# Kernel optimization log

Measured on AMD Instinct MI355X. Metric: run time of the kernel, lower is better.

Reference implementation:

```python
import jax, jax.numpy as jnp
import numpy as np
import math

B, S = 1, 2048
HID = 2048
H = 16
Q_LORA = 1536
KV_LORA = 512
ROPE_D = 64
NOPE_D = 128
V_D = 128
Q_HD = NOPE_D + ROPE_D  # 192
THETA = 10000.0
EPS = 1e-6


def rmsnorm(x, w):
    xf = x.astype(jnp.float32)
    n = xf * jax.lax.rsqrt(jnp.mean(xf * xf, axis=-1, keepdims=True) + EPS)
    return n.astype(x.dtype) * w


def rotate_half(x):
    d = x.shape[-1] // 2
    return jnp.concatenate([-x[..., d:], x[..., :d]], axis=-1)


def setup_inputs() -> dict:
    key = jax.random.key(0)
    ks = jax.random.split(key, 8)
    std = 0.02
    x = jax.random.normal(ks[0], (B, S, HID), dtype=jnp.float32)
    position = jnp.broadcast_to(jnp.arange(S, dtype=jnp.int32), (B, S))
    mask = jnp.broadcast_to(jnp.tril(jnp.ones((S, S), dtype=jnp.int32)), (B, S, S))
    Wq_down = jax.random.normal(ks[1], (HID, Q_LORA), dtype=jnp.float32) * std
    q_norm_w = jnp.ones((Q_LORA,), dtype=jnp.float32)
    Wq_up = jax.random.normal(ks[2], (Q_LORA, H * Q_HD), dtype=jnp.float32) * std
    Wkv_down = jax.random.normal(ks[3], (HID, KV_LORA + ROPE_D), dtype=jnp.float32) * std
    kv_norm_w = jnp.ones((KV_LORA,), dtype=jnp.float32)
    Wkv_up = jax.random.normal(ks[4], (KV_LORA, H * (NOPE_D + V_D)), dtype=jnp.float32) * std
    Wout = jax.random.normal(ks[5], (HID, HID), dtype=jnp.float32) * std
    return {"x": x, "position": position, "mask": mask,
            "Wq_down": Wq_down, "q_norm_w": q_norm_w, "Wq_up": Wq_up,
            "Wkv_down": Wkv_down, "kv_norm_w": kv_norm_w, "Wkv_up": Wkv_up,
            "Wout": Wout}


def reference(x, position, mask, Wq_down, q_norm_w, Wq_up, Wkv_down, kv_norm_w, Wkv_up, Wout):
    b, s, _ = x.shape
    # --- Q path: low-rank down -> RMSNorm -> up ---
    q = rmsnorm(x @ Wq_down, q_norm_w) @ Wq_up            # [B,S,H*Q_HD]
    q = q.reshape(b, s, H, Q_HD).transpose(0, 2, 1, 3)    # [B,H,S,Q_HD]
    q_nope, q_rope = q[..., :NOPE_D], q[..., NOPE_D:]
    # --- KV path ---
    c = x @ Wkv_down                                       # [B,S,KV_LORA+ROPE_D]
    c_kv, k_rope = c[..., :KV_LORA], c[..., KV_LORA:]
    kv = rmsnorm(c_kv, kv_norm_w) @ Wkv_up                 # [B,S,H*(NOPE_D+V_D)]
    kv = kv.reshape(b, s, H, NOPE_D + V_D).transpose(0, 2, 1, 3)
    k_nope, v_state = kv[..., :NOPE_D], kv[..., NOPE_D:]
    k_rope = k_rope[:, None]                               # [B,1,S,ROPE_D]
    # --- RoPE (decoupled, on rope dims only) ---
    inv_freq = 1.0 / (THETA ** (jnp.arange(0, ROPE_D, 2, dtype=jnp.float32) / ROPE_D))
    t = jnp.arange(s, dtype=jnp.float32)
    freqs = jnp.outer(t, inv_freq)                         # [S,ROPE_D/2]
    emb = jnp.concatenate([freqs, freqs], axis=-1)         # [S,ROPE_D]
    cos = jnp.cos(emb)[position][:, None]                  # [B,1,S,ROPE_D]
    sin = jnp.sin(emb)[position][:, None]
    q_rope = q_rope * cos + rotate_half(q_rope) * sin      # [B,H,S,ROPE_D]
    k_rope = k_rope * cos + rotate_half(k_rope) * sin      # [B,1,S,ROPE_D]
    k_rope = jnp.broadcast_to(k_rope, (b, H, s, ROPE_D))
    q_state = jnp.concatenate([q_nope, q_rope], axis=-1)   # [B,H,S,Q_HD]
    k_state = jnp.concatenate([k_nope, k_rope], axis=-1)   # [B,H,S,Q_HD]
    # --- attention (note: original scales by sqrt(v_head_dim)) ---
    scores = jnp.einsum('bhqd,bhkd->bhqk', q_state, k_state) / math.sqrt(V_D)
    scores = jnp.where(mask[:, None] == 0, -jnp.inf, scores)
    att_w = jax.nn.softmax(scores, axis=-1)
    att = jnp.einsum('bhqk,bhkd->bhqd', att_w, v_state)    # [B,H,S,V_D]
    att = att.transpose(0, 2, 1, 3).reshape(b, s, H * V_D) # [B,S,HID]
    return att @ Wout
```

## Files before the change

### kernel.cpp

```cpp
#include <hip/hip_runtime.h>
#include <hip/hip_bf16.h>
#include <math.h>

typedef __bf16 bf16_t;
typedef __bf16 bf16x4 __attribute__((ext_vector_type(4)));
typedef __bf16 bf16x8 __attribute__((ext_vector_type(8)));
typedef float f32x4 __attribute__((ext_vector_type(4)));

#define LOG2E 1.4426950408889634f

typedef const __attribute__((address_space(1))) void* as1cv;
typedef __attribute__((address_space(3))) void* as3v;

__device__ __forceinline__ void gload16(const bf16_t* g, bf16_t* l) {
  __builtin_amdgcn_global_load_lds((as1cv)g, (as3v)l, 16, 0, 0);
}

__global__ __launch_bounds__(256)
void prep_k(const float* __restrict__ x, const float* __restrict__ Wqd,
            const float* __restrict__ Wkvd, const float* __restrict__ Wqu,
            const float* __restrict__ Wkvu, const float* __restrict__ Wout,
            bf16_t* __restrict__ xb, bf16_t* __restrict__ WdT,
            bf16_t* __restrict__ WquT, bf16_t* __restrict__ WkvuT,
            bf16_t* __restrict__ WoutT) {
  __shared__ float t[32][33];
  const int tid = threadIdx.x;
  int bid = blockIdx.x;
  if (bid < 4096) {
    int i = (bid * 256 + tid) * 4;
    float4 v = *(const float4*)(x + i);
    bf16x4 o;
    o[0] = (bf16_t)v.x; o[1] = (bf16_t)v.y; o[2] = (bf16_t)v.z; o[3] = (bf16_t)v.w;
    *(bf16x4*)(xb + i) = o;
    return;
  }
  bid -= 4096;
  const float* in; bf16_t* out; int C, R, bx, by;
  if (bid < 3072)       { in = Wqd;  out = WdT;           R = 2048; C = 1536; bx = bid % 48;  by = bid / 48; }
  else if (bid < 4224)  { int b = bid - 3072;  in = Wkvd; out = WdT + 3145728; R = 2048; C = 576;  bx = b % 18;  by = b / 18; }
  else if (bid < 8832)  { int b = bid - 4224;  in = Wqu;  out = WquT;  R = 1536; C = 3072; bx = b % 96;  by = b / 96; }
  else if (bid < 10880) { int b = bid - 8832;  in = Wkvu; out = WkvuT; R = 512;  C = 4096; bx = b % 128; by = b / 128; }
  else                  { int b = bid - 10880; in = Wout; out = WoutT; R = 2048; C = 2048; bx = b % 64;  by = b / 64; }
  const int c0 = bx * 32, r0 = by * 32;
  const int tx = tid & 31, ty = tid >> 5;
#pragma unroll
  for (int i = 0; i < 32; i += 8)
    t[ty + i][tx] = in[(size_t)(r0 + ty + i) * C + c0 + tx];
  __syncthreads();
#pragma unroll
  for (int i = 0; i < 32; i += 8)
    out[(size_t)(c0 + ty + i) * R + r0 + tx] = (bf16_t)t[tx][ty + i];
}


__device__ __forceinline__ void stage8(const bf16_t* __restrict__ A,
                                       const bf16_t* __restrict__ Bt,
                                       int K, int N, int m0, int n0, int k0,
                                       bf16_t* As, bf16_t* Bs,
                                       int wave, int srow, int scol) {
#pragma unroll
  for (int i = 0; i < 2; ++i) {
    int r0 = (wave * 2 + i) * 8;
    gload16(A + (size_t)(m0 + r0 + srow) * K + k0 + scol, As + r0 * 64);
    int br = n0 + r0 + srow;
    if (br >= N) br = N - 1;
    gload16(Bt + (size_t)br * K + k0 + scol, Bs + r0 * 64);
  }
}

__device__ __forceinline__ void compute8(const bf16_t* As, const bf16_t* Bs,
                                         f32x4 (&acc)[2][4],
                                         int lane, int wr, int wc) {
  const int lm = lane & 15;
  const int sw = lm & 7;
#pragma unroll
  for (int ks = 0; ks < 2; ++ks) {
    const int ck = ((lane >> 4) + ks * 4) ^ sw;
    bf16x8 af[2], bfr[4];
#pragma unroll
    for (int i = 0; i < 2; ++i)
      af[i] = *(const bf16x8*)(As + (wr + i * 16 + lm) * 64 + ck * 8);
#pragma unroll
    for (int i = 0; i < 4; ++i)
      bfr[i] = *(const bf16x8*)(Bs + (wc + i * 16 + lm) * 64 + ck * 8);
#pragma unroll
    for (int mi = 0; mi < 2; ++mi)
#pragma unroll
      for (int ni = 0; ni < 4; ++ni)
        acc[mi][ni] = __builtin_amdgcn_mfma_f32_16x16x32_bf16(
            af[mi], bfr[ni], acc[mi][ni], 0, 0, 0);
  }
}

#define VMCNT(n) asm volatile("s_waitcnt vmcnt(" #n ")" ::: "memory")

__device__ __forceinline__ void gemm128_dbuf8(const bf16_t* __restrict__ A,
                                              const bf16_t* __restrict__ Bt,
                                              int K, int N, int m0, int n0,
                                              bf16_t* lds, f32x4 (&acc)[2][4],
                                              int wave, int lane) {
  const int srow = lane >> 3;
  const int scol = ((lane & 7) ^ srow) * 8;
  const int wr = (wave >> 1) * 32, wc = (wave & 1) * 64;
  bf16_t* A0 = lds;
  bf16_t* B0 = lds + 8192;
  bf16_t* A1 = lds + 16384;
  bf16_t* B1 = lds + 24576;
  const int nk = K >> 6;
  stage8(A, Bt, K, N, m0, n0, 0, A0, B0, wave, srow, scol);
  stage8(A, Bt, K, N, m0, n0, 64, A1, B1, wave, srow, scol);
  VMCNT(4);
  __builtin_amdgcn_s_barrier();
#pragma unroll 1
  for (int t = 0; t < nk; t += 2) {
    compute8(A0, B0, acc, lane, wr, wc);
    __builtin_amdgcn_s_barrier();
    if (t + 2 < nk) {
      stage8(A, Bt, K, N, m0, n0, (t + 2) << 6, A0, B0, wave, srow, scol);
      VMCNT(4);
    } else {
      VMCNT(0);
    }
    __builtin_amdgcn_s_barrier();
    compute8(A1, B1, acc, lane, wr, wc);
    if (t + 3 <= nk) {
      __builtin_amdgcn_s_barrier();
      if (t + 3 < nk) {
        stage8(A, Bt, K, N, m0, n0, (t + 3) << 6, A1, B1, wave, srow, scol);
        VMCNT(4);
      } else {
        VMCNT(0);
      }
      __builtin_amdgcn_s_barrier();
    }
  }
}

__global__ __launch_bounds__(512)
void gemm_dn8(const bf16_t* __restrict__ A, const bf16_t* __restrict__ Bt,
              bf16_t* __restrict__ C, int M, int N, int K) {
  __shared__ __align__(16) bf16_t lds[32768];
  const int tid = threadIdx.x;
  const int wave = tid >> 6, lane = tid & 63;
  const int m0 = blockIdx.y * 128, n0 = blockIdx.x * 128;
  const int wr = (wave >> 1) * 32, wc = (wave & 1) * 64;
  f32x4 acc[2][4] = {};
  gemm128_dbuf8(A, Bt, K, N, m0, n0, lds, acc, wave, lane);
  const int lm = lane & 15, lr = (lane >> 4) * 4;
#pragma unroll
  for (int mi = 0; mi < 2; ++mi)
#pragma unroll
    for (int ni = 0; ni < 4; ++ni) {
      int col = n0 + wc + ni * 16 + lm;
      if (col < N) {
#pragma unroll
        for (int i = 0; i < 4; ++i) {
          int row = m0 + wr + mi * 16 + lr + i;
          C[(size_t)row * N + col] = (bf16_t)acc[mi][ni][i];
        }
      }
    }
}

__global__ __launch_bounds__(512)
void gemm_outf8(const bf16_t* __restrict__ A, const bf16_t* __restrict__ Bt,
                float* __restrict__ C, int M, int N, int K) {
  __shared__ __align__(16) bf16_t lds[32768];
  const int tid = threadIdx.x;
  const int wave = tid >> 6, lane = tid & 63;
  const int m0 = blockIdx.y * 128, n0 = blockIdx.x * 128;
  const int wr = (wave >> 1) * 32, wc = (wave & 1) * 64;
  f32x4 acc[2][4] = {};
  gemm128_dbuf8(A, Bt, K, N, m0, n0, lds, acc, wave, lane);
  const int lm = lane & 15, lr = (lane >> 4) * 4;
#pragma unroll
  for (int mi = 0; mi < 2; ++mi)
#pragma unroll
    for (int ni = 0; ni < 4; ++ni) {
      int col = n0 + wc + ni * 16 + lm;
#pragma unroll
      for (int i = 0; i < 4; ++i) {
        int row = m0 + wr + mi * 16 + lr + i;
        C[(size_t)row * N + col] = acc[mi][ni][i];
      }
    }
}

__global__ __launch_bounds__(512)
void gemm_qkvup8(const bf16_t* __restrict__ qdn, const bf16_t* __restrict__ WquT,
                 const bf16_t* __restrict__ ckvn, const bf16_t* __restrict__ WkvuT,
                 const int* __restrict__ pos, bf16_t* __restrict__ qs,
                 bf16_t* __restrict__ ks, bf16_t* __restrict__ vt) {
  __shared__ __align__(16) bf16_t lds[32768];
  const int tid = threadIdx.x;
  const int wave = tid >> 6, lane = tid & 63;
  const int m0 = blockIdx.y * 128;
  const int wr = (wave >> 1) * 32, wc = (wave & 1) * 64;
  const int lm = lane & 15, lr = (lane >> 4) * 4;
  f32x4 acc[2][4] = {};
  if (blockIdx.x < 24) {
    const int n0 = blockIdx.x * 128;
    gemm128_dbuf8(qdn, WquT, 1536, 3072, m0, n0, lds, acc, wave, lane);
    const bool rope = (((n0 + wc) / 64) % 3) == 2;
    if (rope) {
#pragma unroll
      for (int mi = 0; mi < 2; ++mi)
#pragma unroll
        for (int i = 0; i < 4; ++i) {
          int row = m0 + wr + mi * 16 + lr + i;
          float p = (float)pos[row];
#pragma unroll
          for (int nl = 0; nl < 2; ++nl) {
            int fi = nl * 16 + lm;
            float ang = p * exp2f(-(float)fi * 0.41524101186092030f);
            float sn, cs;
            sincosf(ang, &sn, &cs);
            float v0 = acc[mi][nl][i], v1 = acc[mi][nl + 2][i];
            int c = n0 + wc + nl * 16 + lm;
            int h = c / 192, d = c - h * 192;
            bf16_t* base = qs + ((size_t)h * 2048 + row) * 192;
            base[d]      = (bf16_t)(v0 * cs - v1 * sn);
            base[d + 32] = (bf16_t)(v1 * cs + v0 * sn);
          }
        }
    } else {
#pragma unroll
      for (int mi = 0; mi < 2; ++mi)
#pragma unroll
        for (int ni = 0; ni < 4; ++ni) {
          int c = n0 + wc + ni * 16 + lm;
          int h = c / 192, d = c - h * 192;
#pragma unroll
          for (int i = 0; i < 4; ++i) {
            int row = m0 + wr + mi * 16 + lr + i;
            qs[((size_t)h * 2048 + row) * 192 + d] = (bf16_t)acc[mi][ni][i];
          }
        }
    }
  } else {
    const int n0 = (blockIdx.x - 24) * 128;
    gemm128_dbuf8(ckvn, WkvuT, 512, 4096, m0, n0, lds, acc, wave, lane);
#pragma unroll
    for (int mi = 0; mi < 2; ++mi)
#pragma unroll
      for (int ni = 0; ni < 4; ++ni) {
        int c = n0 + wc + ni * 16 + lm;
        int h = c >> 8, j = c & 255;
#pragma unroll
        for (int i = 0; i < 4; ++i) {
          int row = m0 + wr + mi * 16 + lr + i;
          bf16_t v = (bf16_t)acc[mi][ni][i];
          if (j < 128)
            ks[((size_t)h * 2048 + row) * 192 + j] = v;
          else
            vt[((size_t)h * 128 + (j - 128)) * 2048 + row] = v;
        }
      }
  }
}

__global__ __launch_bounds__(256)
void normrope_k(const bf16_t* __restrict__ Cd, const float* __restrict__ qnw,
                const float* __restrict__ kvnw, const int* __restrict__ pos,
                bf16_t* __restrict__ qdn, bf16_t* __restrict__ ckvn,
                bf16_t* __restrict__ ks) {
  __shared__ float red[4];
  const int bid = blockIdx.x, tid = threadIdx.x;
  if (bid < 4096) {
    const bf16_t* xr;
    const float* W;
    bf16_t* yr;
    int C;
    if (bid < 2048) {
      xr = Cd + (size_t)bid * 2112; W = qnw; yr = qdn + (size_t)bid * 1536; C = 1536;
    } else {
      int r = bid - 2048;
      xr = Cd + (size_t)r * 2112 + 1536; W = kvnw; yr = ckvn + (size_t)r * 512; C = 512;
    }
    int nch = C >> 3;
    bool act = tid < nch;
    float xv[8];
    float ss = 0.f;
    if (act) {
      bf16x8 v = *(const bf16x8*)(xr + tid * 8);
#pragma unroll
      for (int i = 0; i < 8; ++i) { xv[i] = (float)v[i]; ss += xv[i] * xv[i]; }
    }
#pragma unroll
    for (int off = 1; off < 64; off <<= 1) ss += __shfl_xor(ss, off, 64);
    if ((tid & 63) == 0) red[tid >> 6] = ss;
    __syncthreads();
    float tot = red[0] + red[1] + red[2] + red[3];
    float rs = rsqrtf(tot / (float)C + 1e-6f);
    if (act) {
      bf16x8 o;
#pragma unroll
      for (int i = 0; i < 8; ++i) {
        bf16_t nb = (bf16_t)(xv[i] * rs);
        o[i] = (bf16_t)((float)nb * W[tid * 8 + i]);
      }
      *(bf16x8*)(yr + tid * 8) = o;
    }
  } else {
    int s = bid - 4096, d = tid;
    if (d < 64) {
      float v = (float)Cd[(size_t)s * 2112 + 2048 + d];
      int fi = d & 31;
      float p = (float)pos[s];
      float ang = p * exp2f(-(float)fi * 0.415241011860920295f);
      float sn = sinf(ang), co = cosf(ang);
      float other = (float)Cd[(size_t)s * 2112 + 2048 + (d < 32 ? d + 32 : d - 32)];
      v = (d < 32) ? v * co - other * sn : v * co + other * sn;
      bf16_t bv = (bf16_t)v;
#pragma unroll
      for (int h = 0; h < 16; ++h)
        ks[((size_t)h * 2048 + s) * 192 + 128 + d] = bv;
    }
  }
}

__global__ __launch_bounds__(256)
void attn3_k(const bf16_t* __restrict__ Q, const bf16_t* __restrict__ Kst,
             const bf16_t* __restrict__ Vt, bf16_t* __restrict__ O) {
  __shared__ __align__(16) bf16_t Ks[64 * 192];
  __shared__ __align__(16) bf16_t Vs[144 * 64];
  __shared__ __align__(16) bf16_t Ps[4][16 * 72];
  const int bid = blockIdx.x + (blockIdx.y << 5);
  const int lo = bid & 255;
  const int h = lo >> 4;
  const int j = lo & 15;
  const int t = (bid >> 8) ? j : 31 - j;
  const int q0 = t * 64;
  const int nk = t + 1;
  const int tid = threadIdx.x, wave = tid >> 6, lane = tid & 63;
  const int lm = lane & 15, lg = lane >> 4;
  const bf16_t* Qh = Q + (size_t)h * 2048 * 192;
  const bf16_t* Kh = Kst + (size_t)h * 2048 * 192;
  const bf16_t* Vh = Vt + (size_t)h * 128 * 2048;
  const float sc = 0.08838834764831845f * LOG2E;

  bf16x8 aq[6];
#pragma unroll
  for (int tt = 0; tt < 6; ++tt)
    aq[tt] = *(const bf16x8*)(Qh + (size_t)(q0 + wave * 16 + lm) * 192 + tt * 32 + lg * 8);

#pragma unroll
  for (int jj = 0; jj < 4; ++jj) {
    int idx = jj * 256 + tid;
    Vs[128 * 64 + idx] = (bf16_t)(idx < 64 ? 1.0f : 0.0f);
  }

  int kr[6], kc8[6], vr[4], vc8[4];
#pragma unroll
  for (int jj = 0; jj < 6; ++jj) {
    int s = (wave * 6 + jj) * 64 + lane;
    kr[jj] = s / 24;
    kc8[jj] = ((s % 24) ^ (kr[jj] & 7)) * 8;
  }
#pragma unroll
  for (int jj = 0; jj < 4; ++jj) {
    int s = (wave * 4 + jj) * 64 + lane;
    vr[jj] = s >> 3;
    vc8[jj] = ((s & 7) ^ (vr[jj] & 7)) * 8;
  }

  bf16x8 kstg[6], vstg[4];
#pragma unroll
  for (int jj = 0; jj < 6; ++jj)
    kstg[jj] = *(const bf16x8*)(Kh + (size_t)kr[jj] * 192 + kc8[jj]);
#pragma unroll
  for (int jj = 0; jj < 4; ++jj)
    vstg[jj] = *(const bf16x8*)(Vh + (size_t)vr[jj] * 2048 + vc8[jj]);

  f32x4 o[9] = {};

  for (int kt = 0; kt < nk; ++kt) {
    const int k0 = kt * 64;
    if (kt) __syncthreads();
#pragma unroll
    for (int jj = 0; jj < 6; ++jj)
      *(bf16x8*)(Ks + ((wave * 6 + jj) * 64 + lane) * 8) = kstg[jj];
#pragma unroll
    for (int jj = 0; jj < 4; ++jj)
      *(bf16x8*)(Vs + ((wave * 4 + jj) * 64 + lane) * 8) = vstg[jj];
    __syncthreads();

    if (kt + 1 < nk) {
      const int k1 = k0 + 64;
#pragma unroll
      for (int jj = 0; jj < 6; ++jj)
        kstg[jj] = *(const bf16x8*)(Kh + (size_t)(k1 + kr[jj]) * 192 + kc8[jj]);
#pragma unroll
      for (int jj = 0; jj < 4; ++jj)
        vstg[jj] = *(const bf16x8*)(Vh + (size_t)vr[jj] * 2048 + k1 + vc8[jj]);
    }

    f32x4 sa[4] = {};
    __builtin_amdgcn_s_setprio(1);
#pragma unroll
    for (int ct = 0; ct < 4; ++ct) {
#pragma unroll
      for (int tt = 0; tt < 6; ++tt) {
        int cc = (tt * 4 + lg) ^ (lm & 7);
        bf16x8 bk = *(const bf16x8*)(Ks + (ct * 16 + lm) * 192 + cc * 8);
        sa[ct] = __builtin_amdgcn_mfma_f32_16x16x32_bf16(aq[tt], bk, sa[ct], 0, 0, 0);
      }
    }
    __builtin_amdgcn_s_setprio(0);

    bf16_t* Pw = Ps[wave];
    const bool diag = (kt == nk - 1);
#pragma unroll
    for (int i = 0; i < 4; ++i) {
      const int row = q0 + wave * 16 + lg * 4 + i;
#pragma unroll
      for (int ct = 0; ct < 4; ++ct) {
        float p = exp2f(sa[ct][i] * sc);
        if (diag && (k0 + ct * 16 + lm > row)) p = 0.f;
        Pw[(lg * 4 + i) * 72 + ct * 16 + lm] = (bf16_t)p;
      }
    }
    __builtin_amdgcn_s_waitcnt(0xC07F);

    __builtin_amdgcn_s_setprio(1);
#pragma unroll
    for (int ks2 = 0; ks2 < 2; ++ks2) {
      bf16x8 ap = *(const bf16x8*)(Pw + lm * 72 + ks2 * 32 + lg * 8);
#pragma unroll
      for (int nt = 0; nt < 9; ++nt) {
        int rowv = nt * 16 + lm;
        int cc = (ks2 * 4 + lg) ^ (lm & 7);
        bf16x8 bv = *(const bf16x8*)(Vs + rowv * 64 + cc * 8);
        o[nt] = __builtin_amdgcn_mfma_f32_16x16x32_bf16(ap, bv, o[nt], 0, 0, 0);
      }
    }
    __builtin_amdgcn_s_setprio(0);
  }

#pragma unroll
  for (int i = 0; i < 4; ++i) {
    float l = __shfl(o[8][i], (lane & 48), 64);
    float inv = 1.f / l;
    int row = q0 + wave * 16 + lg * 4 + i;
#pragma unroll
    for (int nt = 0; nt < 8; ++nt)
      O[(size_t)row * 2048 + h * 128 + nt * 16 + lm] = (bf16_t)(o[nt][i] * inv);
  }
}

extern "C" void kernel_launch(void* const* d_in, const int* in_sizes, int n_in,
                              void* d_out, int out_size, void* d_ws, size_t ws_size,
                              hipStream_t stream) {
  const float* x    = (const float*)d_in[0];
  const int*   pos  = (const int*)d_in[1];
  const float* Wqd  = (const float*)d_in[3];
  const float* qnw  = (const float*)d_in[4];
  const float* Wqu  = (const float*)d_in[5];
  const float* Wkvd = (const float*)d_in[6];
  const float* kvnw = (const float*)d_in[7];
  const float* Wkvu = (const float*)d_in[8];
  const float* Wout = (const float*)d_in[9];
  float* out = (float*)d_out;

  bf16_t* arena = (bf16_t*)d_ws;
  bf16_t* xb    = arena;
  bf16_t* attb  = arena;
  bf16_t* WdT   = arena + 4194304;
  bf16_t* qdn   = arena + 4194304;
  bf16_t* WquT  = arena + 8519680;
  bf16_t* WkvuT = arena + 13238272;
  bf16_t* WoutT = arena + 15335424;
  bf16_t* Cdown = arena + 19529728;
  bf16_t* vt    = arena + 19529728;
  bf16_t* qs    = arena + 23855104;
  bf16_t* ks    = arena + 30146560;
  bf16_t* ckvn  = arena + 36438016;

  prep_k<<<dim3(19072), 256, 0, stream>>>(x, Wqd, Wkvd, Wqu, Wkvu, Wout,
                                          xb, WdT, WquT, WkvuT, WoutT);

  gemm_dn8<<<dim3(17, 16), 512, 0, stream>>>(xb, WdT, Cdown, 2048, 2112, 2048);

  normrope_k<<<dim3(6144), 256, 0, stream>>>(Cdown, qnw, kvnw, pos, qdn, ckvn, ks);

  gemm_qkvup8<<<dim3(56, 16), 512, 0, stream>>>(qdn, WquT, ckvn, WkvuT, pos,
                                                qs, ks, vt);

  attn3_k<<<dim3(32, 16), 256, 0, stream>>>(qs, ks, vt, attb);

  gemm_outf8<<<dim3(16, 16), 512, 0, stream>>>(attb, WoutT, out, 2048, 2048, 2048);
}
```

Before: 315.6 us.

## Split long causal attention tiles across two blocks with fp32 partial combine

Query tiles 16-31 now have their key range split at tile 16 across two blocks. Each block writes unnormalized fp32 partial outputs and row sums to a workspace buffer, and a new combine kernel adds the two halves and normalizes. Tiles 0-15 still run in one block and write directly. The aim is a more even per-block workload under the causal mask, with 768 blocks instead of 512. In exchange it adds a kernel launch and a round trip of partials through global memory. The partials are combined without a max shift, which is safe only because the kernel already skips max subtraction.

```diff
diff --git a/kernel.cpp b/kernel.cpp
--- a/kernel.cpp
+++ b/kernel.cpp
@@ -321,17 +321,21 @@
 
 __global__ __launch_bounds__(256)
 void attn3_k(const bf16_t* __restrict__ Q, const bf16_t* __restrict__ Kst,
-             const bf16_t* __restrict__ Vt, bf16_t* __restrict__ O) {
+             const bf16_t* __restrict__ Vt, bf16_t* __restrict__ O,
+             float* __restrict__ pbuf) {
   __shared__ __align__(16) bf16_t Ks[64 * 192];
   __shared__ __align__(16) bf16_t Vs[144 * 64];
   __shared__ __align__(16) bf16_t Ps[4][16 * 72];
-  const int bid = blockIdx.x + (blockIdx.y << 5);
+  const int bid = blockIdx.x + (blockIdx.y << 8);
   const int lo = bid & 255;
   const int h = lo >> 4;
-  const int j = lo & 15;
-  const int t = (bid >> 8) ? j : 31 - j;
+  const int jj = lo & 15;
+  int t, kbeg, kend, sp = 0, pidx = 0;
+  bool direct = false;
+  if (bid < 256)      { t = 16 + jj; kbeg = 0;  kend = 16;    sp = 0; pidx = jj; }
+  else if (bid < 512) { t = jj;      kbeg = 0;  kend = t + 1; direct = true; }
+  else                { t = 31 - jj; kbeg = 16; kend = t + 1; sp = 1; pidx = 15 - jj; }
   const int q0 = t * 64;
-  const int nk = t + 1;
   const int tid = threadIdx.x, wave = tid >> 6, lane = tid & 63;
   const int lm = lane & 15, lg = lane >> 4;
   const bf16_t* Qh = Q + (size_t)h * 2048 * 192;
@@ -345,54 +349,55 @@
     aq[tt] = *(const bf16x8*)(Qh + (size_t)(q0 + wave * 16 + lm) * 192 + tt * 32 + lg * 8);
 
 #pragma unroll
-  for (int jj = 0; jj < 4; ++jj) {
-    int idx = jj * 256 + tid;
+  for (int w = 0; w < 4; ++w) {
+    int idx = w * 256 + tid;
     Vs[128 * 64 + idx] = (bf16_t)(idx < 64 ? 1.0f : 0.0f);
   }
 
   int kr[6], kc8[6], vr[4], vc8[4];
 #pragma unroll
-  for (int jj = 0; jj < 6; ++jj) {
-    int s = (wave * 6 + jj) * 64 + lane;
-    kr[jj] = s / 24;
-    kc8[jj] = ((s % 24) ^ (kr[jj] & 7)) * 8;
-  }
-#pragma unroll
-  for (int jj = 0; jj < 4; ++jj) {
-    int s = (wave * 4 + jj) * 64 + lane;
-    vr[jj] = s >> 3;
-    vc8[jj] = ((s & 7) ^ (vr[jj] & 7)) * 8;
+  for (int w = 0; w < 6; ++w) {
+    int s = (wave * 6 + w) * 64 + lane;
+    kr[w] = s / 24;
+    kc8[w] = ((s % 24) ^ (kr[w] & 7)) * 8;
+  }
+#pragma unroll
+  for (int w = 0; w < 4; ++w) {
+    int s = (wave * 4 + w) * 64 + lane;
+    vr[w] = s >> 3;
+    vc8[w] = ((s & 7) ^ (vr[w] & 7)) * 8;
   }
 
   bf16x8 kstg[6], vstg[4];
-#pragma unroll
-  for (int jj = 0; jj < 6; ++jj)
-    kstg[jj] = *(const bf16x8*)(Kh + (size_t)kr[jj] * 192 + kc8[jj]);
-#pragma unroll
-  for (int jj = 0; jj < 4; ++jj)
-    vstg[jj] = *(const bf16x8*)(Vh + (size_t)vr[jj] * 2048 + vc8[jj]);
+  const int kb0 = kbeg * 64;
+#pragma unroll
+  for (int w = 0; w < 6; ++w)
+    kstg[w] = *(const bf16x8*)(Kh + (size_t)(kb0 + kr[w]) * 192 + kc8[w]);
+#pragma unroll
+  for (int w = 0; w < 4; ++w)
+    vstg[w] = *(const bf16x8*)(Vh + (size_t)vr[w] * 2048 + kb0 + vc8[w]);
 
   f32x4 o[9] = {};
 
-  for (int kt = 0; kt < nk; ++kt) {
+  for (int kt = kbeg; kt < kend; ++kt) {
     const int k0 = kt * 64;
-    if (kt) __syncthreads();
-#pragma unroll
-    for (int jj = 0; jj < 6; ++jj)
-      *(bf16x8*)(Ks + ((wave * 6 + jj) * 64 + lane) * 8) = kstg[jj];
-#pragma unroll
-    for (int jj = 0; jj < 4; ++jj)
-      *(bf16x8*)(Vs + ((wave * 4 + jj) * 64 + lane) * 8) = vstg[jj];
+    if (kt != kbeg) __syncthreads();
+#pragma unroll
+    for (int w = 0; w < 6; ++w)
+      *(bf16x8*)(Ks + ((wave * 6 + w) * 64 + lane) * 8) = kstg[w];
+#pragma unroll
+    for (int w = 0; w < 4; ++w)
+      *(bf16x8*)(Vs + ((wave * 4 + w) * 64 + lane) * 8) = vstg[w];
     __syncthreads();
 
-    if (kt + 1 < nk) {
+    if (kt + 1 < kend) {
       const int k1 = k0 + 64;
 #pragma unroll
-      for (int jj = 0; jj < 6; ++jj)
-        kstg[jj] = *(const bf16x8*)(Kh + (size_t)(k1 + kr[jj]) * 192 + kc8[jj]);
-#pragma unroll
-      for (int jj = 0; jj < 4; ++jj)
-        vstg[jj] = *(const bf16x8*)(Vh + (size_t)vr[jj] * 2048 + k1 + vc8[jj]);
+      for (int w = 0; w < 6; ++w)
+        kstg[w] = *(const bf16x8*)(Kh + (size_t)(k1 + kr[w]) * 192 + kc8[w]);
+#pragma unroll
+      for (int w = 0; w < 4; ++w)
+        vstg[w] = *(const bf16x8*)(Vh + (size_t)vr[w] * 2048 + k1 + vc8[w]);
     }
 
     f32x4 sa[4] = {};
@@ -409,7 +414,7 @@
     __builtin_amdgcn_s_setprio(0);
 
     bf16_t* Pw = Ps[wave];
-    const bool diag = (kt == nk - 1);
+    const bool diag = (kt == t);
 #pragma unroll
     for (int i = 0; i < 4; ++i) {
       const int row = q0 + wave * 16 + lg * 4 + i;
@@ -437,14 +442,49 @@
     __builtin_amdgcn_s_setprio(0);
   }
 
-#pragma unroll
-  for (int i = 0; i < 4; ++i) {
-    float l = __shfl(o[8][i], (lane & 48), 64);
-    float inv = 1.f / l;
-    int row = q0 + wave * 16 + lg * 4 + i;
-#pragma unroll
-    for (int nt = 0; nt < 8; ++nt)
-      O[(size_t)row * 2048 + h * 128 + nt * 16 + lm] = (bf16_t)(o[nt][i] * inv);
+  if (direct) {
+#pragma unroll
+    for (int i = 0; i < 4; ++i) {
+      float l = __shfl(o[8][i], (lane & 48), 64);
+      float inv = 1.f / l;
+      int row = q0 + wave * 16 + lg * 4 + i;
+#pragma unroll
+      for (int nt = 0; nt < 8; ++nt)
+        O[(size_t)row * 2048 + h * 128 + nt * 16 + lm] = (bf16_t)(o[nt][i] * inv);
+    }
+  } else {
+    float* P = pbuf + ((size_t)(h * 16 + pidx) * 2 + sp) * 8448;
+#pragma unroll
+    for (int i = 0; i < 4; ++i) {
+      int r = wave * 16 + lg * 4 + i;
+#pragma unroll
+      for (int nt = 0; nt < 8; ++nt)
+        P[r * 132 + nt * 16 + lm] = o[nt][i];
+      if (lm == 0) P[r * 132 + 128] = o[8][i];
+    }
+  }
+}
+
+__global__ __launch_bounds__(256)
+void combine_k(const float* __restrict__ pbuf, bf16_t* __restrict__ O) {
+  const int b = blockIdx.x, tid = threadIdx.x;
+  const int h = b >> 4, pidx = b & 15;
+  const int r = tid >> 2, c0 = (tid & 3) * 32;
+  const float* p0 = pbuf + ((size_t)(h * 16 + pidx) * 2) * 8448 + r * 132;
+  const float* p1 = p0 + 8448;
+  const float inv = 1.f / (p0[128] + p1[128]);
+  const int row = (16 + pidx) * 64 + r;
+  bf16_t* dst = O + (size_t)row * 2048 + h * 128 + c0;
+#pragma unroll
+  for (int i = 0; i < 32; i += 4) {
+    float4 a = *(const float4*)(p0 + c0 + i);
+    float4 c = *(const float4*)(p1 + c0 + i);
+    bf16x4 v;
+    v[0] = (bf16_t)((a.x + c.x) * inv);
+    v[1] = (bf16_t)((a.y + c.y) * inv);
+    v[2] = (bf16_t)((a.z + c.z) * inv);
+    v[3] = (bf16_t)((a.w + c.w) * inv);
+    *(bf16x4*)(dst + i) = v;
   }
 }
 
@@ -469,6 +509,7 @@
   bf16_t* qdn   = arena + 4194304;
   bf16_t* WquT  = arena + 8519680;
   bf16_t* WkvuT = arena + 13238272;
+  float*  pbuf  = (float*)(arena + 4194304);
   bf16_t* WoutT = arena + 15335424;
   bf16_t* Cdown = arena + 19529728;
   bf16_t* vt    = arena + 19529728;
@@ -486,7 +527,9 @@
   gemm_qkvup8<<<dim3(56, 16), 512, 0, stream>>>(qdn, WquT, ckvn, WkvuT, pos,
                                                 qs, ks, vt);
 
-  attn3_k<<<dim3(32, 16), 256, 0, stream>>>(qs, ks, vt, attb);
+  attn3_k<<<dim3(256, 3), 256, 0, stream>>>(qs, ks, vt, attb, pbuf);
+
+  combine_k<<<dim3(256), 256, 0, stream>>>(pbuf, attb);
 
   gemm_outf8<<<dim3(16, 16), 512, 0, stream>>>(attb, WoutT, out, 2048, 2048, 2048);
 }
```

Result: no change. 310.6 us (-1.6%).
